# Optimization experiments

Measured on AMD Instinct MI355X. Metric: run time of the kernel, lower is better.

## Reference

```python
import jax, jax.numpy as jnp
import numpy as np

N = 32768
DEG = 9        # 8 neighbors + self-loop
B = 8
K = 3          # Chebyshev degree
IN_CH = 8
OUT_CH = 2
HID = 64


def setup_inputs() -> dict:
    key = jax.random.key(0)
    ks = jax.random.split(key, 14)
    # structured 9-neighbor stencil (CSR-like sorted rows), honoring graph sparsity
    offs = np.arange(-4, 5)
    rows_np = np.repeat(np.arange(N), DEG).astype(np.int32)
    cols_np = ((rows_np.reshape(N, DEG) + offs[None, :]) % N).reshape(-1).astype(np.int32)
    vals = jax.random.normal(ks[0], (N * DEG,), jnp.float32) * 0.1
    x = jax.random.normal(ks[1], (B, N, IN_CH), jnp.float32)

    def w(k, fin, fout):
        return jax.random.normal(k, (K * fin, fout), jnp.float32) * 0.05

    def b(k, fout):
        return jax.random.normal(k, (fout,), jnp.float32) * 0.01

    return dict(
        x=x, rows=jnp.asarray(rows_np), cols=jnp.asarray(cols_np), vals=vals,
        W1=w(ks[2], IN_CH, HID), b1=b(ks[3], HID),
        W2=w(ks[4], HID, HID), b2=b(ks[5], HID),
        W3=w(ks[6], HID, HID), b3=b(ks[7], HID),
        W4=w(ks[8], HID, HID), b4=b(ks[9], HID),
        W5=w(ks[10], HID, OUT_CH), b5=b(ks[11], OUT_CH),
    )


def _spmm(rows, cols, vals, x):
    # sparse Laplacian @ x ; x: [B, N, C] -> [B, N, C]
    g = x[:, cols, :] * vals[None, :, None]          # [B, nnz, C]
    g = jnp.swapaxes(g, 0, 1)                        # [nnz, B, C]
    y = jax.ops.segment_sum(g, rows, num_segments=N) # [N, B, C]
    return jnp.swapaxes(y, 0, 1)


def _cheb_conv(rows, cols, vals, x, W, b):
    # Chebyshev recursion: T0 = x, T1 = L x, Tk = 2 L T_{k-1} - T_{k-2}
    x0 = x
    xs = [x0]
    if K > 1:
        x1 = _spmm(rows, cols, vals, x0)
        xs.append(x1)
        for _ in range(K - 2):
            x2 = 2.0 * _spmm(rows, cols, vals, x1) - x0
            xs.append(x2)
            x0, x1 = x1, x2
    xk = jnp.concatenate(xs, axis=-1)                # [B, N, K*Fin]
    return jnp.einsum('bnf,fo->bno', xk, W) + b


def reference(x, rows, cols, vals, W1, b1, W2, b2, W3, b3, W4, b4, W5, b5):
    h = jax.nn.elu(_cheb_conv(rows, cols, vals, x, W1, b1))
    h = jax.nn.elu(_cheb_conv(rows, cols, vals, h, W2, b2))
    h = jax.nn.elu(_cheb_conv(rows, cols, vals, h, W3, b3))
    h = jax.nn.elu(_cheb_conv(rows, cols, vals, h, W4, b4))
    out = _cheb_conv(rows, cols, vals, h, W5, b5)    # no ELU on last layer
    return out
```

## Files before the change

### kernel.cpp

```cpp
#include <hip/hip_runtime.h>
#include <math.h>

#define N_PIX 32768
#define DEG 9
#define BATCH 8
#define TILE 64

typedef __attribute__((ext_vector_type(8))) short bf16x8;
typedef __attribute__((ext_vector_type(16))) float f32x16;

__device__ __forceinline__ unsigned short bf16_rn(float x) {
    unsigned int u = __builtin_bit_cast(unsigned int, x);
    u += 0x7fffu + ((u >> 16) & 1u);
    return (unsigned short)(u >> 16);
}
__device__ __forceinline__ float bf16_to_f(unsigned short u) {
    unsigned int v = ((unsigned int)u) << 16;
    return __builtin_bit_cast(float, v);
}

__global__ void prep_wt(const float* __restrict__ W2, const float* __restrict__ W3,
                        const float* __restrict__ W4, unsigned short* __restrict__ out) {
    const float* W = (blockIdx.x == 0) ? W2 : (blockIdx.x == 1) ? W3 : W4;
    unsigned short* o = out + (size_t)blockIdx.x * 24576;
    const int base = blockIdx.y * 768;
    for (int idx = base + threadIdx.x; idx < base + 768; idx += 256) {
        int j = idx & 7;
        int lane = (idx >> 3) & 63;
        int rest = idx >> 9;
        int s = rest % 12, t = rest / 12;
        int k = s * 16 + (lane >> 5) * 8 + j;
        int n = t * 32 + (lane & 31);
        float x = W[k * 64 + n];
        unsigned short hi = bf16_rn(x);
        unsigned short lo = bf16_rn(x - bf16_to_f(hi));
        o[idx] = hi;
        o[12288 + idx] = lo;
    }
}

__global__ __launch_bounds__(512, 4)
void cheb_mid2(const float* __restrict__ X, const float* __restrict__ vals,
               const unsigned short* __restrict__ Wt, const float* __restrict__ bias,
               float* __restrict__ Y) {
    __shared__ alignas(16) float Xs[80 * 68];
    __shared__ alignas(16) float T1[72 * 68];
    __shared__ alignas(16) float T2[64 * 68];
    __shared__ alignas(16) float Vs[648];
    __shared__ float Bs[64];

    const int tid = threadIdx.x;
    const int n0 = blockIdx.x * TILE;
    const int b  = blockIdx.y;
    const float* Xb = X + (size_t)b * N_PIX * 64;

    if (tid < 64) Bs[tid] = bias[tid];
    for (int i = tid; i < 1280; i += 512) {
        int r = i >> 4, c = (i & 15) << 2;
        int g = (n0 - 8 + r) & (N_PIX - 1);
        *(float4*)&Xs[r * 68 + c] = *(const float4*)&Xb[(size_t)g * 64 + c];
    }
    for (int i = tid; i < 648; i += 512) {
        int v = i / 9;
        int g = (n0 - 4 + v) & (N_PIX - 1);
        Vs[i] = vals[(size_t)g * DEG + (i - v * 9)];
    }
    __syncthreads();

    if (tid < 384) {
        const int st = tid >> 4, f0 = (tid & 15) << 2;
        const int r0 = st * 3;
        float4 xw[11];
        #pragma unroll
        for (int l = 0; l < 11; ++l)
            xw[l] = *(const float4*)&Xs[(r0 + l) * 68 + f0];
        #pragma unroll
        for (int r = 0; r < 3; ++r) {
            float4 a = {0.f, 0.f, 0.f, 0.f};
            #pragma unroll
            for (int j = 0; j < DEG; ++j) {
                float vj = Vs[(r0 + r) * 9 + j];
                float4 xv = xw[r + j];
                a.x = fmaf(vj, xv.x, a.x); a.y = fmaf(vj, xv.y, a.y);
                a.z = fmaf(vj, xv.z, a.z); a.w = fmaf(vj, xv.w, a.w);
            }
            *(float4*)&T1[(r0 + r) * 68 + f0] = a;
        }
    }
    __syncthreads();

    {
        const int st = tid >> 4, f0 = (tid & 15) << 2;
        const int r0 = st * 2;
        float4 tw[10];
        #pragma unroll
        for (int l = 0; l < 10; ++l)
            tw[l] = *(const float4*)&T1[(r0 + l) * 68 + f0];
        #pragma unroll
        for (int r = 0; r < 2; ++r) {
            float4 a = {0.f, 0.f, 0.f, 0.f};
            #pragma unroll
            for (int j = 0; j < DEG; ++j) {
                float vj = Vs[(r0 + r + 4) * 9 + j];
                float4 xv = tw[r + j];
                a.x = fmaf(vj, xv.x, a.x); a.y = fmaf(vj, xv.y, a.y);
                a.z = fmaf(vj, xv.z, a.z); a.w = fmaf(vj, xv.w, a.w);
            }
            float4 x0 = *(const float4*)&Xs[(r0 + r + 8) * 68 + f0];
            a.x = 2.f * a.x - x0.x; a.y = 2.f * a.y - x0.y;
            a.z = 2.f * a.z - x0.z; a.w = 2.f * a.w - x0.w;
            *(float4*)&T2[(r0 + r) * 68 + f0] = a;
        }
    }
    __syncthreads();

    {
        const int w = tid >> 6, lane = tid & 63;
        const int t = w & 3, kh = w >> 2;
        const int rh = t >> 1, ch = t & 1;
        const int m = lane & 31, half = lane >> 5;
        const int rt = rh * 32 + m;
        f32x16 acc = {};
        #pragma unroll
        for (int u = 0; u < 6; ++u) {
            const int s = kh * 6 + u;
            const int k0 = s * 16 + half * 8;
            const float* src;
            if (k0 < 64)       src = &Xs[(rt + 8) * 68 + k0];
            else if (k0 < 128) src = &T1[(rt + 4) * 68 + (k0 - 64)];
            else               src = &T2[rt * 68 + (k0 - 128)];
            float4 xa = *(const float4*)src;
            float4 xb = *(const float4*)(src + 4);
            float xf[8] = {xa.x, xa.y, xa.z, xa.w, xb.x, xb.y, xb.z, xb.w};
            bf16x8 ah, al;
            #pragma unroll
            for (int e = 0; e < 8; ++e) {
                unsigned short h = bf16_rn(xf[e]);
                ah[e] = (short)h;
                al[e] = (short)bf16_rn(xf[e] - bf16_to_f(h));
            }
            const int widx = ((ch * 12 + s) * 64 + lane) * 8;
            bf16x8 bh = *(const bf16x8*)&Wt[widx];
            bf16x8 bl = *(const bf16x8*)&Wt[12288 + widx];
            acc = __builtin_amdgcn_mfma_f32_32x32x16_bf16(al, bh, acc, 0, 0, 0);
            acc = __builtin_amdgcn_mfma_f32_32x32x16_bf16(ah, bl, acc, 0, 0, 0);
            acc = __builtin_amdgcn_mfma_f32_32x32x16_bf16(ah, bh, acc, 0, 0, 0);
        }
        float* Red = Xs;
        __syncthreads();
        if (kh == 1) {
            #pragma unroll
            for (int rg = 0; rg < 16; ++rg) Red[(t * 16 + rg) * 64 + lane] = acc[rg];
        }
        __syncthreads();
        if (kh == 0) {
            const int col = ch * 32 + m;
            float* Yb = Y + ((size_t)b * N_PIX + n0) * 64;
            #pragma unroll
            for (int rg = 0; rg < 16; ++rg) {
                int row = rh * 32 + (rg & 3) + 8 * (rg >> 2) + 4 * half;
                float v = acc[rg] + Red[(t * 16 + rg) * 64 + lane] + Bs[col];
                v = v > 0.f ? v : expm1f(v);
                Yb[(size_t)row * 64 + col] = v;
            }
        }
    }
}

__global__ __launch_bounds__(512, 4)
void cheb_last(const float* __restrict__ X, const float* __restrict__ vals,
               const float* __restrict__ W5, const float* __restrict__ b5,
               float* __restrict__ Y) {
    __shared__ alignas(16) float Xs[80 * 68];
    __shared__ alignas(16) float Wst[384];
    __shared__ alignas(16) float Pb[80 * 8];
    __shared__ alignas(16) float Sb[72 * 4];
    __shared__ alignas(16) float Vs[648];
    __shared__ float Bs[2];

    const int tid = threadIdx.x;
    const int n0 = blockIdx.x * TILE;
    const int b  = blockIdx.y;
    const float* Xb = X + (size_t)b * N_PIX * 64;

    if (tid < 2) Bs[tid] = b5[tid];
    if (tid < 384) { int k = tid >> 1, o = tid & 1; Wst[o * 192 + k] = W5[tid]; }
    for (int i = tid; i < 1280; i += 512) {
        int r = i >> 4, c = (i & 15) << 2;
        int g = (n0 - 8 + r) & (N_PIX - 1);
        *(float4*)&Xs[r * 68 + c] = *(const float4*)&Xb[(size_t)g * 64 + c];
    }
    for (int i = tid; i < 648; i += 512) {
        int v = i / 9;
        int g = (n0 - 4 + v) & (N_PIX - 1);
        Vs[i] = vals[(size_t)g * DEG + (i - v * 9)];
    }
    __syncthreads();

    if (tid < 480) {
        const int r = tid / 6, rem = tid - r * 6;
        const int s = rem >> 1, o = rem & 1;
        const float* wcol = &Wst[o * 192 + s * 64];
        float acc = 0.f;
        #pragma unroll 4
        for (int q = 0; q < 16; ++q) {
            float4 xv = *(const float4*)&Xs[r * 68 + q * 4];
            float4 wv = *(const float4*)&wcol[q * 4];
            acc = fmaf(xv.x, wv.x, acc); acc = fmaf(xv.y, wv.y, acc);
            acc = fmaf(xv.z, wv.z, acc); acc = fmaf(xv.w, wv.w, acc);
        }
        Pb[r * 8 + s * 2 + o] = acc;
    }
    __syncthreads();

    if (tid < 144) {
        const int sr = tid >> 1, o = tid & 1;
        float q = 0.f;
        #pragma unroll
        for (int j = 0; j < DEG; ++j)
            q = fmaf(Vs[sr * 9 + j], Pb[(sr + j) * 8 + 4 + o], q);
        Sb[sr * 4 + o] = Pb[(sr + 4) * 8 + 2 + o] + 2.f * q;
    }
    __syncthreads();

    if (tid < 128) {
        const int r = tid >> 1, o = tid & 1;
        float q = 0.f;
        #pragma unroll
        for (int j = 0; j < DEG; ++j)
            q = fmaf(Vs[(r + 4) * 9 + j], Sb[(r + j) * 4 + o], q);
        float v = Pb[(r + 8) * 8 + o] - Pb[(r + 8) * 8 + 4 + o] + q + Bs[o];
        Y[((size_t)b * N_PIX + n0 + r) * 2 + o] = v;
    }
}

__global__ __launch_bounds__(512, 8)
void cheb_first(const float* __restrict__ X, const float* __restrict__ vals,
                const float* __restrict__ W, const float* __restrict__ bias,
                float* __restrict__ Y) {
    constexpr int LDA = 12;
    __shared__ alignas(16) float Xs[80 * LDA];
    __shared__ alignas(16) float T1s[72 * LDA];
    __shared__ alignas(16) float T2s[64 * LDA];
    __shared__ alignas(16) float Ws[24 * 64];
    __shared__ alignas(16) float Red[256 * 16];
    __shared__ float Bs[64];

    const int tid = threadIdx.x;
    const int n0 = blockIdx.x * TILE;
    const int b  = blockIdx.y;

    for (int i = tid; i < 24 * 64; i += 512) Ws[i] = W[i];
    if (tid < 64) Bs[tid] = bias[tid];

    const float* Xb = X + (size_t)b * N_PIX * 8;
    for (int i = tid; i < 160; i += 512) {
        int r = i >> 1, h = (i & 1) << 2;
        int g = (n0 - 8 + r) & (N_PIX - 1);
        *(float4*)&Xs[r * LDA + h] = *(const float4*)&Xb[(size_t)g * 8 + h];
    }
    __syncthreads();

    if (tid < 144) {
        int r = tid >> 1, h = (tid & 1) << 2;
        int g = (n0 - 4 + r) & (N_PIX - 1);
        const float* vr = vals + (size_t)g * DEG;
        float4 a = {0.f, 0.f, 0.f, 0.f};
        #pragma unroll
        for (int j = 0; j < DEG; ++j) {
            float vj = vr[j];
            float4 xv = *(const float4*)&Xs[(r + j) * LDA + h];
            a.x = fmaf(vj, xv.x, a.x); a.y = fmaf(vj, xv.y, a.y);
            a.z = fmaf(vj, xv.z, a.z); a.w = fmaf(vj, xv.w, a.w);
        }
        *(float4*)&T1s[r * LDA + h] = a;
    }
    __syncthreads();

    if (tid < 128) {
        int r = tid >> 1, h = (tid & 1) << 2;
        const float* vr = vals + (size_t)(n0 + r) * DEG;
        float4 a = {0.f, 0.f, 0.f, 0.f};
        #pragma unroll
        for (int j = 0; j < DEG; ++j) {
            float vj = vr[j];
            float4 xv = *(const float4*)&T1s[(r + j) * LDA + h];
            a.x = fmaf(vj, xv.x, a.x); a.y = fmaf(vj, xv.y, a.y);
            a.z = fmaf(vj, xv.z, a.z); a.w = fmaf(vj, xv.w, a.w);
        }
        float4 x0 = *(const float4*)&Xs[(r + 8) * LDA + h];
        a.x = 2.f * a.x - x0.x; a.y = 2.f * a.y - x0.y;
        a.z = 2.f * a.z - x0.z; a.w = 2.f * a.w - x0.w;
        *(float4*)&T2s[r * LDA + h] = a;
    }
    __syncthreads();

    {
        const int g   = tid >> 8;
        const int lid = tid & 255;
        const int ty = lid >> 4, tx = lid & 15;
        const int r0 = ty * 4, c0 = tx * 4;
        float acc[4][4] = {};
        const float* tbs[3] = { Xs + 8 * LDA, T1s + 4 * LDA, T2s };
        #pragma unroll
        for (int s = 0; s < 3; ++s) {
            const float* T = tbs[s];
            const float* Wseg = Ws + s * 8 * 64;
            const int f0 = g * 4;
            float a[4][4];
            #pragma unroll
            for (int i = 0; i < 4; ++i)
                *(float4*)(a[i]) = *(const float4*)(T + (r0 + i) * LDA + f0);
            #pragma unroll
            for (int k = 0; k < 4; ++k) {
                float wv[4];
                *(float4*)wv = *(const float4*)(Wseg + (f0 + k) * 64 + c0);
                #pragma unroll
                for (int i = 0; i < 4; ++i)
                    #pragma unroll
                    for (int j = 0; j < 4; ++j)
                        acc[i][j] = fmaf(a[i][k], wv[j], acc[i][j]);
            }
        }
        if (g == 1) {
            float* dst = Red + lid * 16;
            #pragma unroll
            for (int i = 0; i < 4; ++i)
                #pragma unroll
                for (int j = 0; j < 4; ++j) dst[i * 4 + j] = acc[i][j];
        }
        __syncthreads();
        if (g == 0) {
            const float* src = Red + lid * 16;
            float* Yb = Y + ((size_t)b * N_PIX + n0) * 64;
            #pragma unroll
            for (int i = 0; i < 4; ++i) {
                float vv[4];
                #pragma unroll
                for (int j = 0; j < 4; ++j) {
                    float t = acc[i][j] + src[i * 4 + j] + Bs[c0 + j];
                    t = t > 0.f ? t : expm1f(t);
                    vv[j] = t;
                }
                *(float4*)(Yb + (size_t)(r0 + i) * 64 + c0) = *(const float4*)vv;
            }
        }
    }
}

extern "C" void kernel_launch(void* const* d_in, const int* in_sizes, int n_in,
                              void* d_out, int out_size, void* d_ws, size_t ws_size,
                              hipStream_t stream) {
    const float* x    = (const float*)d_in[0];
    const float* vals = (const float*)d_in[3];
    const float* W1 = (const float*)d_in[4];
    const float* b1 = (const float*)d_in[5];
    const float* W2 = (const float*)d_in[6];
    const float* b2 = (const float*)d_in[7];
    const float* W3 = (const float*)d_in[8];
    const float* b3 = (const float*)d_in[9];
    const float* W4 = (const float*)d_in[10];
    const float* b4 = (const float*)d_in[11];
    const float* W5 = (const float*)d_in[12];
    const float* b5 = (const float*)d_in[13];
    float* out = (float*)d_out;

    float* bufA = (float*)d_ws;
    float* bufB = bufA + (size_t)BATCH * N_PIX * 64;

    unsigned short* wt = (unsigned short*)d_out;

    dim3 grid(N_PIX / TILE, BATCH);
    prep_wt<<<dim3(3, 16), dim3(256), 0, stream>>>(W2, W3, W4, wt);
    cheb_first<<<grid, dim3(512), 0, stream>>>(x, vals, W1, b1, bufA);
    cheb_mid2<<<grid, dim3(512), 0, stream>>>(bufA, vals, wt,         b2, bufB);
    cheb_mid2<<<grid, dim3(512), 0, stream>>>(bufB, vals, wt + 24576, b3, bufA);
    cheb_mid2<<<grid, dim3(512), 0, stream>>>(bufA, vals, wt + 49152, b4, bufB);
    cheb_last<<<grid, dim3(512), 0, stream>>>(bufB, vals, W5, b5, out);
}
```

Before: 358.6 us.

## Apply weights before the Laplacian and store activations as split bf16 pairs

Each Chebyshev layer is reordered so the dense weight GEMM runs first on the raw input via MFMA. The result is combined as P0 + L(P1 + 2 L P2), with the W0-W2 difference folded into the weights. This removes the per-tile fp32-to-bf16 splitting of T1/T2 before the MFMA, and the sparse stencil now works on already-projected features. Inter-layer activations are stored as bf16 hi/lo planes in a swizzled LDS layout, so they can be fed to the MFMA directly. The cost is extra halo rows in the GEMM, redundant recomputation over overlapping rows, and a change in rounding order.

```diff
diff --git a/kernel.cpp b/kernel.cpp
--- a/kernel.cpp
+++ b/kernel.cpp
@@ -6,85 +6,163 @@
 #define BATCH 8
 #define TILE 64
 
+typedef unsigned short u16;
 typedef __attribute__((ext_vector_type(8))) short bf16x8;
 typedef __attribute__((ext_vector_type(16))) float f32x16;
 
-__device__ __forceinline__ unsigned short bf16_rn(float x) {
+__device__ __forceinline__ u16 bf16_rn(float x) {
     unsigned int u = __builtin_bit_cast(unsigned int, x);
     u += 0x7fffu + ((u >> 16) & 1u);
-    return (unsigned short)(u >> 16);
-}
-__device__ __forceinline__ float bf16_to_f(unsigned short u) {
+    return (u16)(u >> 16);
+}
+__device__ __forceinline__ float bf16_to_f(u16 u) {
     unsigned int v = ((unsigned int)u) << 16;
     return __builtin_bit_cast(float, v);
 }
 
 __global__ void prep_wt(const float* __restrict__ W2, const float* __restrict__ W3,
-                        const float* __restrict__ W4, unsigned short* __restrict__ out) {
+                        const float* __restrict__ W4, u16* __restrict__ out) {
     const float* W = (blockIdx.x == 0) ? W2 : (blockIdx.x == 1) ? W3 : W4;
-    unsigned short* o = out + (size_t)blockIdx.x * 24576;
+    u16* o = out + (size_t)blockIdx.x * 24576;
     const int base = blockIdx.y * 768;
     for (int idx = base + threadIdx.x; idx < base + 768; idx += 256) {
         int j = idx & 7;
         int lane = (idx >> 3) & 63;
         int rest = idx >> 9;
-        int s = rest % 12, t = rest / 12;
+        int s = rest & 3, tt = rest >> 2;
+        int t = tt & 1, mat = tt >> 1;
         int k = s * 16 + (lane >> 5) * 8 + j;
         int n = t * 32 + (lane & 31);
-        float x = W[k * 64 + n];
-        unsigned short hi = bf16_rn(x);
-        unsigned short lo = bf16_rn(x - bf16_to_f(hi));
+        float x = (mat == 0) ? W[k * 64 + n] - W[(128 + k) * 64 + n]
+                : (mat == 1) ? W[(64 + k) * 64 + n]
+                             : W[(128 + k) * 64 + n];
+        u16 hi = bf16_rn(x);
         o[idx] = hi;
-        o[12288 + idx] = lo;
+        o[12288 + idx] = bf16_rn(x - bf16_to_f(hi));
     }
 }
 
 __global__ __launch_bounds__(512, 4)
-void cheb_mid2(const float* __restrict__ X, const float* __restrict__ vals,
-               const unsigned short* __restrict__ Wt, const float* __restrict__ bias,
-               float* __restrict__ Y) {
-    __shared__ alignas(16) float Xs[80 * 68];
-    __shared__ alignas(16) float T1[72 * 68];
-    __shared__ alignas(16) float T2[64 * 68];
-    __shared__ alignas(16) float Vs[648];
-    __shared__ float Bs[64];
+void cheb_mid3(const u16* __restrict__ Xh, const u16* __restrict__ Xl,
+               const float* __restrict__ vals, const u16* __restrict__ Wt,
+               const float* __restrict__ bias,
+               u16* __restrict__ Yh, u16* __restrict__ Yl) {
+    __shared__ alignas(16) u16 Ah[80 * 64];
+    __shared__ alignas(16) u16 Al[80 * 64];
+    __shared__ alignas(16) float P2s[80 * 68];
+    __shared__ alignas(16) float P1s[72 * 64];
+    __shared__ alignas(16) float P0s[64 * 65];
+    __shared__ alignas(16) float Vs[72 * 12];
 
     const int tid = threadIdx.x;
     const int n0 = blockIdx.x * TILE;
     const int b  = blockIdx.y;
-    const float* Xb = X + (size_t)b * N_PIX * 64;
-
-    if (tid < 64) Bs[tid] = bias[tid];
-    for (int i = tid; i < 1280; i += 512) {
-        int r = i >> 4, c = (i & 15) << 2;
+    const u16* XhB = Xh + (size_t)b * N_PIX * 64;
+    const u16* XlB = Xl + (size_t)b * N_PIX * 64;
+
+    for (int i = tid; i < 640; i += 512) {
+        int r = i >> 3, cb = i & 7;
         int g = (n0 - 8 + r) & (N_PIX - 1);
-        *(float4*)&Xs[r * 68 + c] = *(const float4*)&Xb[(size_t)g * 64 + c];
+        int d = r * 64 + ((cb ^ (r & 7)) << 3);
+        *(uint4*)&Ah[d] = *(const uint4*)&XhB[(size_t)g * 64 + cb * 8];
+        *(uint4*)&Al[d] = *(const uint4*)&XlB[(size_t)g * 64 + cb * 8];
     }
     for (int i = tid; i < 648; i += 512) {
-        int v = i / 9;
-        int g = (n0 - 4 + v) & (N_PIX - 1);
-        Vs[i] = vals[(size_t)g * DEG + (i - v * 9)];
+        int sr = i / 9, j = i - sr * 9;
+        int g = (n0 - 4 + sr) & (N_PIX - 1);
+        Vs[sr * 12 + j] = vals[(size_t)g * DEG + j];
+    }
+    __syncthreads();
+
+    {
+        const int w = tid >> 6, lane = tid & 63;
+        const int m = lane & 31, half = lane >> 5;
+        if (w < 6) {
+            const int t = w & 1, mi_idx = w >> 1;
+            const int mi = (mi_idx == 2) ? 48 : mi_idx * 32;
+            const int row = mi + m;
+            f32x16 acc1 = {}, acc2 = {};
+            #pragma unroll
+            for (int s = 0; s < 4; ++s) {
+                int cb = s * 2 + half;
+                int off = row * 64 + ((cb ^ (row & 7)) << 3);
+                bf16x8 ah = *(const bf16x8*)&Ah[off];
+                bf16x8 al = *(const bf16x8*)&Al[off];
+                const u16* w1p = &Wt[((2 + t) * 4 + s) * 512 + lane * 8];
+                const u16* w2p = &Wt[((4 + t) * 4 + s) * 512 + lane * 8];
+                bf16x8 b1h = *(const bf16x8*)w1p;
+                bf16x8 b1l = *(const bf16x8*)(w1p + 12288);
+                bf16x8 b2h = *(const bf16x8*)w2p;
+                bf16x8 b2l = *(const bf16x8*)(w2p + 12288);
+                acc1 = __builtin_amdgcn_mfma_f32_32x32x16_bf16(al, b1h, acc1, 0, 0, 0);
+                acc1 = __builtin_amdgcn_mfma_f32_32x32x16_bf16(ah, b1l, acc1, 0, 0, 0);
+                acc1 = __builtin_amdgcn_mfma_f32_32x32x16_bf16(ah, b1h, acc1, 0, 0, 0);
+                acc2 = __builtin_amdgcn_mfma_f32_32x32x16_bf16(al, b2h, acc2, 0, 0, 0);
+                acc2 = __builtin_amdgcn_mfma_f32_32x32x16_bf16(ah, b2l, acc2, 0, 0, 0);
+                acc2 = __builtin_amdgcn_mfma_f32_32x32x16_bf16(ah, b2h, acc2, 0, 0, 0);
+            }
+            const int col = t * 32 + m;
+            #pragma unroll
+            for (int rg = 0; rg < 16; ++rg) {
+                int rr = mi + (rg & 3) + 8 * (rg >> 2) + 4 * half;
+                P2s[rr * 68 + col] = acc2[rg];
+                if (rr >= 4 && rr < 76) P1s[(rr - 4) * 64 + col] = acc1[rg];
+            }
+        } else {
+            const int t = w - 6;
+            #pragma unroll
+            for (int item = 0; item < 2; ++item) {
+                const int mi = item ? 40 : 8;
+                const int row = mi + m;
+                f32x16 acc = {};
+                #pragma unroll
+                for (int s = 0; s < 4; ++s) {
+                    int cb = s * 2 + half;
+                    int off = row * 64 + ((cb ^ (row & 7)) << 3);
+                    bf16x8 ah = *(const bf16x8*)&Ah[off];
+                    bf16x8 al = *(const bf16x8*)&Al[off];
+                    const u16* w0p = &Wt[(t * 4 + s) * 512 + lane * 8];
+                    bf16x8 b0h = *(const bf16x8*)w0p;
+                    bf16x8 b0l = *(const bf16x8*)(w0p + 12288);
+                    acc = __builtin_amdgcn_mfma_f32_32x32x16_bf16(al, b0h, acc, 0, 0, 0);
+                    acc = __builtin_amdgcn_mfma_f32_32x32x16_bf16(ah, b0l, acc, 0, 0, 0);
+                    acc = __builtin_amdgcn_mfma_f32_32x32x16_bf16(ah, b0h, acc, 0, 0, 0);
+                }
+                const int col = t * 32 + m;
+                #pragma unroll
+                for (int rg = 0; rg < 16; ++rg) {
+                    int rr = mi + (rg & 3) + 8 * (rg >> 2) + 4 * half;
+                    P0s[(rr - 8) * 65 + col] = acc[rg];
+                }
+            }
+        }
     }
     __syncthreads();
 
     if (tid < 384) {
         const int st = tid >> 4, f0 = (tid & 15) << 2;
-        const int r0 = st * 3;
-        float4 xw[11];
+        float4 win[11];
         #pragma unroll
         for (int l = 0; l < 11; ++l)
-            xw[l] = *(const float4*)&Xs[(r0 + l) * 68 + f0];
+            win[l] = *(const float4*)&P2s[(st * 3 + l) * 68 + f0];
         #pragma unroll
         for (int r = 0; r < 3; ++r) {
+            const int br = st * 3 + r;
+            float4 vA = *(const float4*)&Vs[br * 12];
+            float4 vB = *(const float4*)&Vs[br * 12 + 4];
+            float v8 = Vs[br * 12 + 8];
             float4 a = {0.f, 0.f, 0.f, 0.f};
-            #pragma unroll
-            for (int j = 0; j < DEG; ++j) {
-                float vj = Vs[(r0 + r) * 9 + j];
-                float4 xv = xw[r + j];
-                a.x = fmaf(vj, xv.x, a.x); a.y = fmaf(vj, xv.y, a.y);
-                a.z = fmaf(vj, xv.z, a.z); a.w = fmaf(vj, xv.w, a.w);
-            }
-            *(float4*)&T1[(r0 + r) * 68 + f0] = a;
+            const float vj[9] = {vA.x, vA.y, vA.z, vA.w, vB.x, vB.y, vB.z, vB.w, v8};
+            #pragma unroll
+            for (int j = 0; j < 9; ++j) {
+                float4 xv = win[r + j];
+                a.x = fmaf(vj[j], xv.x, a.x); a.y = fmaf(vj[j], xv.y, a.y);
+                a.z = fmaf(vj[j], xv.z, a.z); a.w = fmaf(vj[j], xv.w, a.w);
+            }
+            float4 p1 = *(const float4*)&P1s[br * 64 + f0];
+            p1.x = fmaf(2.f, a.x, p1.x); p1.y = fmaf(2.f, a.y, p1.y);
+            p1.z = fmaf(2.f, a.z, p1.z); p1.w = fmaf(2.f, a.w, p1.w);
+            *(float4*)&P1s[br * 64 + f0] = p1;
         }
     }
     __syncthreads();
@@ -92,83 +170,210 @@
     {
         const int st = tid >> 4, f0 = (tid & 15) << 2;
         const int r0 = st * 2;
-        float4 tw[10];
+        float4 win[10];
         #pragma unroll
         for (int l = 0; l < 10; ++l)
-            tw[l] = *(const float4*)&T1[(r0 + l) * 68 + f0];
+            win[l] = *(const float4*)&P1s[(r0 + l) * 64 + f0];
+        const float4 bb = *(const float4*)&bias[f0];
         #pragma unroll
         for (int r = 0; r < 2; ++r) {
+            const int br = r0 + r;
+            float4 vA = *(const float4*)&Vs[(br + 4) * 12];
+            float4 vB = *(const float4*)&Vs[(br + 4) * 12 + 4];
+            float v8 = Vs[(br + 4) * 12 + 8];
+            float4 a = bb;
+            const float vj[9] = {vA.x, vA.y, vA.z, vA.w, vB.x, vB.y, vB.z, vB.w, v8};
+            #pragma unroll
+            for (int j = 0; j < 9; ++j) {
+                float4 xv = win[r + j];
+                a.x = fmaf(vj[j], xv.x, a.x); a.y = fmaf(vj[j], xv.y, a.y);
+                a.z = fmaf(vj[j], xv.z, a.z); a.w = fmaf(vj[j], xv.w, a.w);
+            }
+            *(float4*)&P2s[br * 68 + f0] = a;
+        }
+    }
+    __syncthreads();
+
+    {
+        const int r = tid >> 3, c0 = (tid & 7) << 3;
+        float4 qa = *(const float4*)&P2s[r * 68 + c0];
+        float4 qb = *(const float4*)&P2s[r * 68 + c0 + 4];
+        float y[8] = {qa.x, qa.y, qa.z, qa.w, qb.x, qb.y, qb.z, qb.w};
+        #pragma unroll
+        for (int i = 0; i < 8; ++i) {
+            float v = y[i] + P0s[r * 65 + c0 + i];
+            y[i] = v > 0.f ? v : expm1f(v);
+        }
+        unsigned int hw[4], lw[4];
+        #pragma unroll
+        for (int p = 0; p < 4; ++p) {
+            u16 h0 = bf16_rn(y[2 * p]);
+            u16 l0 = bf16_rn(y[2 * p] - bf16_to_f(h0));
+            u16 h1 = bf16_rn(y[2 * p + 1]);
+            u16 l1 = bf16_rn(y[2 * p + 1] - bf16_to_f(h1));
+            hw[p] = (unsigned int)h0 | ((unsigned int)h1 << 16);
+            lw[p] = (unsigned int)l0 | ((unsigned int)l1 << 16);
+        }
+        size_t base = ((size_t)b * N_PIX + n0 + r) * 64 + c0;
+        *(uint4*)&Yh[base] = make_uint4(hw[0], hw[1], hw[2], hw[3]);
+        *(uint4*)&Yl[base] = make_uint4(lw[0], lw[1], lw[2], lw[3]);
+    }
+}
+
+__global__ __launch_bounds__(512, 4)
+void cheb_first2(const float* __restrict__ X, const float* __restrict__ vals,
+                 const float* __restrict__ W, const float* __restrict__ bias,
+                 u16* __restrict__ Yh, u16* __restrict__ Yl) {
+    __shared__ alignas(16) float X8[80 * 12];
+    __shared__ alignas(16) float Wf[24 * 64];
+    __shared__ alignas(16) float W0p[8 * 64];
+    __shared__ alignas(16) float P2s[80 * 68];
+    __shared__ alignas(16) float P1s[72 * 64];
+    __shared__ alignas(16) float P0s[64 * 68];
+    __shared__ alignas(16) float Vs[72 * 12];
+
+    const int tid = threadIdx.x;
+    const int n0 = blockIdx.x * TILE;
+    const int b  = blockIdx.y;
+    const float* Xb = X + (size_t)b * N_PIX * 8;
+
+    for (int i = tid; i < 1536; i += 512) Wf[i] = W[i];
+    for (int i = tid; i < 160; i += 512) {
+        int r = i >> 1, h = (i & 1) << 2;
+        int g = (n0 - 8 + r) & (N_PIX - 1);
+        *(float4*)&X8[r * 12 + h] = *(const float4*)&Xb[(size_t)g * 8 + h];
+    }
+    for (int i = tid; i < 648; i += 512) {
+        int sr = i / 9, j = i - sr * 9;
+        int g = (n0 - 4 + sr) & (N_PIX - 1);
+        Vs[sr * 12 + j] = vals[(size_t)g * DEG + j];
+    }
+    __syncthreads();
+    W0p[tid & 511] = Wf[tid & 511] - Wf[1024 + (tid & 511)];
+    __syncthreads();
+
+    for (int idx = tid; idx < 1280; idx += 512) {
+        int row = idx >> 4, f0 = (idx & 15) << 2;
+        float4 a = {0.f, 0.f, 0.f, 0.f};
+        #pragma unroll
+        for (int k = 0; k < 8; ++k) {
+            float xv = X8[row * 12 + k];
+            float4 wv = *(const float4*)&Wf[(16 + k) * 64 + f0];
+            a.x = fmaf(xv, wv.x, a.x); a.y = fmaf(xv, wv.y, a.y);
+            a.z = fmaf(xv, wv.z, a.z); a.w = fmaf(xv, wv.w, a.w);
+        }
+        *(float4*)&P2s[row * 68 + f0] = a;
+    }
+    for (int idx = tid; idx < 1152; idx += 512) {
+        int br = idx >> 4, f0 = (idx & 15) << 2;
+        float4 a = {0.f, 0.f, 0.f, 0.f};
+        #pragma unroll
+        for (int k = 0; k < 8; ++k) {
+            float xv = X8[(br + 4) * 12 + k];
+            float4 wv = *(const float4*)&Wf[(8 + k) * 64 + f0];
+            a.x = fmaf(xv, wv.x, a.x); a.y = fmaf(xv, wv.y, a.y);
+            a.z = fmaf(xv, wv.z, a.z); a.w = fmaf(xv, wv.w, a.w);
+        }
+        *(float4*)&P1s[br * 64 + f0] = a;
+    }
+    for (int idx = tid; idx < 1024; idx += 512) {
+        int ry = idx >> 4, f0 = (idx & 15) << 2;
+        float4 a = {0.f, 0.f, 0.f, 0.f};
+        #pragma unroll
+        for (int k = 0; k < 8; ++k) {
+            float xv = X8[(ry + 8) * 12 + k];
+            float4 wv = *(const float4*)&W0p[k * 64 + f0];
+            a.x = fmaf(xv, wv.x, a.x); a.y = fmaf(xv, wv.y, a.y);
+            a.z = fmaf(xv, wv.z, a.z); a.w = fmaf(xv, wv.w, a.w);
+        }
+        *(float4*)&P0s[ry * 68 + f0] = a;
+    }
+    __syncthreads();
+
+    if (tid < 384) {
+        const int st = tid >> 4, f0 = (tid & 15) << 2;
+        float4 win[11];
+        #pragma unroll
+        for (int l = 0; l < 11; ++l)
+            win[l] = *(const float4*)&P2s[(st * 3 + l) * 68 + f0];
+        #pragma unroll
+        for (int r = 0; r < 3; ++r) {
+            const int br = st * 3 + r;
+            float4 vA = *(const float4*)&Vs[br * 12];
+            float4 vB = *(const float4*)&Vs[br * 12 + 4];
+            float v8 = Vs[br * 12 + 8];
             float4 a = {0.f, 0.f, 0.f, 0.f};
-            #pragma unroll
-            for (int j = 0; j < DEG; ++j) {
-                float vj = Vs[(r0 + r + 4) * 9 + j];
-                float4 xv = tw[r + j];
-                a.x = fmaf(vj, xv.x, a.x); a.y = fmaf(vj, xv.y, a.y);
-                a.z = fmaf(vj, xv.z, a.z); a.w = fmaf(vj, xv.w, a.w);
-            }
-            float4 x0 = *(const float4*)&Xs[(r0 + r + 8) * 68 + f0];
-            a.x = 2.f * a.x - x0.x; a.y = 2.f * a.y - x0.y;
-            a.z = 2.f * a.z - x0.z; a.w = 2.f * a.w - x0.w;
-            *(float4*)&T2[(r0 + r) * 68 + f0] = a;
+            const float vj[9] = {vA.x, vA.y, vA.z, vA.w, vB.x, vB.y, vB.z, vB.w, v8};
+            #pragma unroll
+            for (int j = 0; j < 9; ++j) {
+                float4 xv = win[r + j];
+                a.x = fmaf(vj[j], xv.x, a.x); a.y = fmaf(vj[j], xv.y, a.y);
+                a.z = fmaf(vj[j], xv.z, a.z); a.w = fmaf(vj[j], xv.w, a.w);
+            }
+            float4 p1 = *(const float4*)&P1s[br * 64 + f0];
+            p1.x = fmaf(2.f, a.x, p1.x); p1.y = fmaf(2.f, a.y, p1.y);
+            p1.z = fmaf(2.f, a.z, p1.z); p1.w = fmaf(2.f, a.w, p1.w);
+            *(float4*)&P1s[br * 64 + f0] = p1;
         }
     }
     __syncthreads();
 
     {
-        const int w = tid >> 6, lane = tid & 63;
-        const int t = w & 3, kh = w >> 2;
-        const int rh = t >> 1, ch = t & 1;
-        const int m = lane & 31, half = lane >> 5;
-        const int rt = rh * 32 + m;
-        f32x16 acc = {};
-        #pragma unroll
-        for (int u = 0; u < 6; ++u) {
-            const int s = kh * 6 + u;
-            const int k0 = s * 16 + half * 8;
-            const float* src;
-            if (k0 < 64)       src = &Xs[(rt + 8) * 68 + k0];
-            else if (k0 < 128) src = &T1[(rt + 4) * 68 + (k0 - 64)];
-            else               src = &T2[rt * 68 + (k0 - 128)];
-            float4 xa = *(const float4*)src;
-            float4 xb = *(const float4*)(src + 4);
-            float xf[8] = {xa.x, xa.y, xa.z, xa.w, xb.x, xb.y, xb.z, xb.w};
-            bf16x8 ah, al;
-            #pragma unroll
-            for (int e = 0; e < 8; ++e) {
-                unsigned short h = bf16_rn(xf[e]);
-                ah[e] = (short)h;
-                al[e] = (short)bf16_rn(xf[e] - bf16_to_f(h));
-            }
-            const int widx = ((ch * 12 + s) * 64 + lane) * 8;
-            bf16x8 bh = *(const bf16x8*)&Wt[widx];
-            bf16x8 bl = *(const bf16x8*)&Wt[12288 + widx];
-            acc = __builtin_amdgcn_mfma_f32_32x32x16_bf16(al, bh, acc, 0, 0, 0);
-            acc = __builtin_amdgcn_mfma_f32_32x32x16_bf16(ah, bl, acc, 0, 0, 0);
-            acc = __builtin_amdgcn_mfma_f32_32x32x16_bf16(ah, bh, acc, 0, 0, 0);
-        }
-        float* Red = Xs;
-        __syncthreads();
-        if (kh == 1) {
-            #pragma unroll
-            for (int rg = 0; rg < 16; ++rg) Red[(t * 16 + rg) * 64 + lane] = acc[rg];
-        }
-        __syncthreads();
-        if (kh == 0) {
-            const int col = ch * 32 + m;
-            float* Yb = Y + ((size_t)b * N_PIX + n0) * 64;
-            #pragma unroll
-            for (int rg = 0; rg < 16; ++rg) {
-                int row = rh * 32 + (rg & 3) + 8 * (rg >> 2) + 4 * half;
-                float v = acc[rg] + Red[(t * 16 + rg) * 64 + lane] + Bs[col];
-                v = v > 0.f ? v : expm1f(v);
-                Yb[(size_t)row * 64 + col] = v;
-            }
-        }
+        const int st = tid >> 4, f0 = (tid & 15) << 2;
+        const int r0 = st * 2;
+        float4 win[10];
+        #pragma unroll
+        for (int l = 0; l < 10; ++l)
+            win[l] = *(const float4*)&P1s[(r0 + l) * 64 + f0];
+        const float4 bb = *(const float4*)&bias[f0];
+        #pragma unroll
+        for (int r = 0; r < 2; ++r) {
+            const int br = r0 + r;
+            float4 vA = *(const float4*)&Vs[(br + 4) * 12];
+            float4 vB = *(const float4*)&Vs[(br + 4) * 12 + 4];
+            float v8 = Vs[(br + 4) * 12 + 8];
+            float4 a = bb;
+            const float vj[9] = {vA.x, vA.y, vA.z, vA.w, vB.x, vB.y, vB.z, vB.w, v8};
+            #pragma unroll
+            for (int j = 0; j < 9; ++j) {
+                float4 xv = win[r + j];
+                a.x = fmaf(vj[j], xv.x, a.x); a.y = fmaf(vj[j], xv.y, a.y);
+                a.z = fmaf(vj[j], xv.z, a.z); a.w = fmaf(vj[j], xv.w, a.w);
+            }
+            *(float4*)&P2s[br * 68 + f0] = a;
+        }
+    }
+    __syncthreads();
+
+    {
+        const int r = tid >> 3, c0 = (tid & 7) << 3;
+        float4 qa = *(const float4*)&P2s[r * 68 + c0];
+        float4 qb = *(const float4*)&P2s[r * 68 + c0 + 4];
+        float4 pa = *(const float4*)&P0s[r * 68 + c0];
+        float4 pb = *(const float4*)&P0s[r * 68 + c0 + 4];
+        float y[8] = {qa.x + pa.x, qa.y + pa.y, qa.z + pa.z, qa.w + pa.w,
+                      qb.x + pb.x, qb.y + pb.y, qb.z + pb.z, qb.w + pb.w};
+        #pragma unroll
+        for (int i = 0; i < 8; ++i) y[i] = y[i] > 0.f ? y[i] : expm1f(y[i]);
+        unsigned int hw[4], lw[4];
+        #pragma unroll
+        for (int p = 0; p < 4; ++p) {
+            u16 h0 = bf16_rn(y[2 * p]);
+            u16 l0 = bf16_rn(y[2 * p] - bf16_to_f(h0));
+            u16 h1 = bf16_rn(y[2 * p + 1]);
+            u16 l1 = bf16_rn(y[2 * p + 1] - bf16_to_f(h1));
+            hw[p] = (unsigned int)h0 | ((unsigned int)h1 << 16);
+            lw[p] = (unsigned int)l0 | ((unsigned int)l1 << 16);
+        }
+        size_t base = ((size_t)b * N_PIX + n0 + r) * 64 + c0;
+        *(uint4*)&Yh[base] = make_uint4(hw[0], hw[1], hw[2], hw[3]);
+        *(uint4*)&Yl[base] = make_uint4(lw[0], lw[1], lw[2], lw[3]);
     }
 }
 
 __global__ __launch_bounds__(512, 4)
-void cheb_last(const float* __restrict__ X, const float* __restrict__ vals,
+void cheb_last(const u16* __restrict__ Xh, const u16* __restrict__ Xl,
+               const float* __restrict__ vals,
                const float* __restrict__ W5, const float* __restrict__ b5,
                float* __restrict__ Y) {
     __shared__ alignas(16) float Xs[80 * 68];
@@ -181,14 +386,24 @@
     const int tid = threadIdx.x;
     const int n0 = blockIdx.x * TILE;
     const int b  = blockIdx.y;
-    const float* Xb = X + (size_t)b * N_PIX * 64;
+    const u16* XhB = Xh + (size_t)b * N_PIX * 64;
+    const u16* XlB = Xl + (size_t)b * N_PIX * 64;
 
     if (tid < 2) Bs[tid] = b5[tid];
     if (tid < 384) { int k = tid >> 1, o = tid & 1; Wst[o * 192 + k] = W5[tid]; }
-    for (int i = tid; i < 1280; i += 512) {
-        int r = i >> 4, c = (i & 15) << 2;
+    for (int i = tid; i < 640; i += 512) {
+        int r = i >> 3, cb = i & 7;
         int g = (n0 - 8 + r) & (N_PIX - 1);
-        *(float4*)&Xs[r * 68 + c] = *(const float4*)&Xb[(size_t)g * 64 + c];
+        const u16* hp = &XhB[(size_t)g * 64 + cb * 8];
+        const u16* lp = &XlB[(size_t)g * 64 + cb * 8];
+        ushort4 h0 = *(const ushort4*)hp, h1 = *(const ushort4*)(hp + 4);
+        ushort4 l0 = *(const ushort4*)lp, l1 = *(const ushort4*)(lp + 4);
+        float4 fa = {bf16_to_f(h0.x) + bf16_to_f(l0.x), bf16_to_f(h0.y) + bf16_to_f(l0.y),
+                     bf16_to_f(h0.z) + bf16_to_f(l0.z), bf16_to_f(h0.w) + bf16_to_f(l0.w)};
+        float4 fb = {bf16_to_f(h1.x) + bf16_to_f(l1.x), bf16_to_f(h1.y) + bf16_to_f(l1.y),
+                     bf16_to_f(h1.z) + bf16_to_f(l1.z), bf16_to_f(h1.w) + bf16_to_f(l1.w)};
+        *(float4*)&Xs[r * 68 + cb * 8] = fa;
+        *(float4*)&Xs[r * 68 + cb * 8 + 4] = fb;
     }
     for (int i = tid; i < 648; i += 512) {
         int v = i / 9;
@@ -231,120 +446,6 @@
             q = fmaf(Vs[(r + 4) * 9 + j], Sb[(r + j) * 4 + o], q);
         float v = Pb[(r + 8) * 8 + o] - Pb[(r + 8) * 8 + 4 + o] + q + Bs[o];
         Y[((size_t)b * N_PIX + n0 + r) * 2 + o] = v;
-    }
-}
-
-__global__ __launch_bounds__(512, 8)
-void cheb_first(const float* __restrict__ X, const float* __restrict__ vals,
-                const float* __restrict__ W, const float* __restrict__ bias,
-                float* __restrict__ Y) {
-    constexpr int LDA = 12;
-    __shared__ alignas(16) float Xs[80 * LDA];
-    __shared__ alignas(16) float T1s[72 * LDA];
-    __shared__ alignas(16) float T2s[64 * LDA];
-    __shared__ alignas(16) float Ws[24 * 64];
-    __shared__ alignas(16) float Red[256 * 16];
-    __shared__ float Bs[64];
-
-    const int tid = threadIdx.x;
-    const int n0 = blockIdx.x * TILE;
-    const int b  = blockIdx.y;
-
-    for (int i = tid; i < 24 * 64; i += 512) Ws[i] = W[i];
-    if (tid < 64) Bs[tid] = bias[tid];
-
-    const float* Xb = X + (size_t)b * N_PIX * 8;
-    for (int i = tid; i < 160; i += 512) {
-        int r = i >> 1, h = (i & 1) << 2;
-        int g = (n0 - 8 + r) & (N_PIX - 1);
-        *(float4*)&Xs[r * LDA + h] = *(const float4*)&Xb[(size_t)g * 8 + h];
-    }
-    __syncthreads();
-
-    if (tid < 144) {
-        int r = tid >> 1, h = (tid & 1) << 2;
-        int g = (n0 - 4 + r) & (N_PIX - 1);
-        const float* vr = vals + (size_t)g * DEG;
-        float4 a = {0.f, 0.f, 0.f, 0.f};
-        #pragma unroll
-        for (int j = 0; j < DEG; ++j) {
-            float vj = vr[j];
-            float4 xv = *(const float4*)&Xs[(r + j) * LDA + h];
-            a.x = fmaf(vj, xv.x, a.x); a.y = fmaf(vj, xv.y, a.y);
-            a.z = fmaf(vj, xv.z, a.z); a.w = fmaf(vj, xv.w, a.w);
-        }
-        *(float4*)&T1s[r * LDA + h] = a;
-    }
-    __syncthreads();
-
-    if (tid < 128) {
-        int r = tid >> 1, h = (tid & 1) << 2;
-        const float* vr = vals + (size_t)(n0 + r) * DEG;
-        float4 a = {0.f, 0.f, 0.f, 0.f};
-        #pragma unroll
-        for (int j = 0; j < DEG; ++j) {
-            float vj = vr[j];
-            float4 xv = *(const float4*)&T1s[(r + j) * LDA + h];
-            a.x = fmaf(vj, xv.x, a.x); a.y = fmaf(vj, xv.y, a.y);
-            a.z = fmaf(vj, xv.z, a.z); a.w = fmaf(vj, xv.w, a.w);
-        }
-        float4 x0 = *(const float4*)&Xs[(r + 8) * LDA + h];
-        a.x = 2.f * a.x - x0.x; a.y = 2.f * a.y - x0.y;
-        a.z = 2.f * a.z - x0.z; a.w = 2.f * a.w - x0.w;
-        *(float4*)&T2s[r * LDA + h] = a;
-    }
-    __syncthreads();
-
-    {
-        const int g   = tid >> 8;
-        const int lid = tid & 255;
-        const int ty = lid >> 4, tx = lid & 15;
-        const int r0 = ty * 4, c0 = tx * 4;
-        float acc[4][4] = {};
-        const float* tbs[3] = { Xs + 8 * LDA, T1s + 4 * LDA, T2s };
-        #pragma unroll
-        for (int s = 0; s < 3; ++s) {
-            const float* T = tbs[s];
-            const float* Wseg = Ws + s * 8 * 64;
-            const int f0 = g * 4;
-            float a[4][4];
-            #pragma unroll
-            for (int i = 0; i < 4; ++i)
-                *(float4*)(a[i]) = *(const float4*)(T + (r0 + i) * LDA + f0);
-            #pragma unroll
-            for (int k = 0; k < 4; ++k) {
-                float wv[4];
-                *(float4*)wv = *(const float4*)(Wseg + (f0 + k) * 64 + c0);
-                #pragma unroll
-                for (int i = 0; i < 4; ++i)
-                    #pragma unroll
-                    for (int j = 0; j < 4; ++j)
-                        acc[i][j] = fmaf(a[i][k], wv[j], acc[i][j]);
-            }
-        }
-        if (g == 1) {
-            float* dst = Red + lid * 16;
-            #pragma unroll
-            for (int i = 0; i < 4; ++i)
-                #pragma unroll
-                for (int j = 0; j < 4; ++j) dst[i * 4 + j] = acc[i][j];
-        }
-        __syncthreads();
-        if (g == 0) {
-            const float* src = Red + lid * 16;
-            float* Yb = Y + ((size_t)b * N_PIX + n0) * 64;
-            #pragma unroll
-            for (int i = 0; i < 4; ++i) {
-                float vv[4];
-                #pragma unroll
-                for (int j = 0; j < 4; ++j) {
-                    float t = acc[i][j] + src[i * 4 + j] + Bs[c0 + j];
-                    t = t > 0.f ? t : expm1f(t);
-                    vv[j] = t;
-                }
-                *(float4*)(Yb + (size_t)(r0 + i) * 64 + c0) = *(const float4*)vv;
-            }
-        }
     }
 }
 
@@ -365,16 +466,18 @@
     const float* b5 = (const float*)d_in[13];
     float* out = (float*)d_out;
 
-    float* bufA = (float*)d_ws;
-    float* bufB = bufA + (size_t)BATCH * N_PIX * 64;
-
-    unsigned short* wt = (unsigned short*)d_out;
+    const size_t PL = (size_t)BATCH * N_PIX * 64;
+    u16* Ah_g = (u16*)d_ws;
+    u16* Al_g = Ah_g + PL;
+    u16* Bh_g = Ah_g + 2 * PL;
+    u16* Bl_g = Ah_g + 3 * PL;
+    u16* wt = (u16*)d_out;
 
     dim3 grid(N_PIX / TILE, BATCH);
     prep_wt<<<dim3(3, 16), dim3(256), 0, stream>>>(W2, W3, W4, wt);
-    cheb_first<<<grid, dim3(512), 0, stream>>>(x, vals, W1, b1, bufA);
-    cheb_mid2<<<grid, dim3(512), 0, stream>>>(bufA, vals, wt,         b2, bufB);
-    cheb_mid2<<<grid, dim3(512), 0, stream>>>(bufB, vals, wt + 24576, b3, bufA);
-    cheb_mid2<<<grid, dim3(512), 0, stream>>>(bufA, vals, wt + 49152, b4, bufB);
-    cheb_last<<<grid, dim3(512), 0, stream>>>(bufB, vals, W5, b5, out);
-}
+    cheb_first2<<<grid, dim3(512), 0, stream>>>(x, vals, W1, b1, Ah_g, Al_g);
+    cheb_mid3<<<grid, dim3(512), 0, stream>>>(Ah_g, Al_g, vals, wt,         b2, Bh_g, Bl_g);
+    cheb_mid3<<<grid, dim3(512), 0, stream>>>(Bh_g, Bl_g, vals, wt + 24576, b3, Ah_g, Al_g);
+    cheb_mid3<<<grid, dim3(512), 0, stream>>>(Ah_g, Al_g, vals, wt + 49152, b4, Bh_g, Bl_g);
+    cheb_last<<<grid, dim3(512), 0, stream>>>(Bh_g, Bl_g, vals, W5, b5, out);
+}
```

After: 345.2 us. 3.7% less time.
